# Performance work log

Hardware: AMD Instinct MI355X
Metric: run time of the kernel (lower is better)

## Reference

```python
import jax, jax.numpy as jnp
import numpy as np

HEADS = 16

def setup_inputs() -> dict:
    key = jax.random.key(0)
    ks = jax.random.split(key, 5)
    B, N, C = 2, 2048, 1024
    s = 0.02
    return {
        "x": jax.random.normal(ks[0], (B, N, C), jnp.float32),
        "y": jax.random.normal(ks[1], (B, N, C), jnp.float32),
        "w_qkv": jax.random.normal(ks[2], (C, 3 * C), jnp.float32) * s,  # acts as Linear weight^T
        "w_proj": jax.random.normal(ks[3], (C, C), jnp.float32) * s,
        "b_proj": jnp.zeros((C,), jnp.float32),
    }

def _qkv_heads(t, w_qkv, B, N, H, D):
    qkv = (t @ w_qkv).reshape(B, N, 3, H, D)
    qkv = jnp.transpose(qkv, (2, 0, 3, 1, 4))  # [3, B, H, N, D]
    return qkv[0], qkv[1], qkv[2]

def reference(x, y, w_qkv, w_proj, b_proj):
    B, N, C = x.shape
    H = HEADS
    D = C // H
    scale = D ** (-0.5)
    q, k, v = _qkv_heads(x, w_qkv, B, N, H, D)
    q1, k1, v1 = _qkv_heads(y, w_qkv, B, N, H, D)
    attn = jax.nn.softmax(jnp.einsum('bhnd,bhmd->bhnm', q, k) * scale, axis=-1)
    attn1 = jax.nn.softmax(jnp.einsum('bhnd,bhmd->bhnm', q1, k1) * scale, axis=-1)
    # cross-swapped values: x-branch attends over v1 (from y), y-branch over v (from x)
    ox = jnp.einsum('bhnm,bhmd->bhnd', attn, v1)
    oy = jnp.einsum('bhnm,bhmd->bhnd', attn1, v)
    ox = jnp.transpose(ox, (0, 2, 1, 3)).reshape(B, N, C)
    oy = jnp.transpose(oy, (0, 2, 1, 3)).reshape(B, N, C)
    x_out = ox @ w_proj + b_proj + x
    y_out = oy @ w_proj + b_proj + y
    return x_out, y_out
```

## Files before the change

kernel.cpp:

```cpp
#include <hip/hip_runtime.h>

using u16    = unsigned short;
using short8 = __attribute__((ext_vector_type(8))) short;
using f32x4  = __attribute__((ext_vector_type(4))) float;

#define MFMA16(a, b, c) __builtin_amdgcn_mfma_f32_16x16x32_bf16(a, b, c, 0, 0, 0)

#define QSCALE 0.18033688011112042f

__device__ inline u16 f2bf(float f) {
  union { float f; unsigned u; } v; v.f = f;
  unsigned r = v.u + 0x7fffu + ((v.u >> 16) & 1u);
  return (u16)(r >> 16);
}

__device__ __forceinline__ void load_lds16(const u16* g, u16* l) {
  __builtin_amdgcn_global_load_lds((const __attribute__((address_space(1))) void*)g,
                                   (__attribute__((address_space(3))) void*)l, 16, 0, 0);
}

__global__ __launch_bounds__(256) void cvt_k(const float* __restrict__ src,
                                             u16* __restrict__ dst) {
  const int i = (blockIdx.x * 256 + threadIdx.x) * 8;
  const float4 a = *(const float4*)&src[i];
  const float4 b = *(const float4*)&src[i + 4];
  short8 o;
  o[0] = (short)f2bf(a.x); o[1] = (short)f2bf(a.y);
  o[2] = (short)f2bf(a.z); o[3] = (short)f2bf(a.w);
  o[4] = (short)f2bf(b.x); o[5] = (short)f2bf(b.y);
  o[6] = (short)f2bf(b.z); o[7] = (short)f2bf(b.w);
  *(short8*)&dst[i] = o;
}

__global__ __launch_bounds__(256) void cvtT_k(const float* __restrict__ src,
                                              u16* __restrict__ dst, int R, int C) {
  __shared__ float t[64][65];
  const int c0 = blockIdx.x * 64, r0 = blockIdx.y * 64;
  const int lc = threadIdx.x & 63, g = threadIdx.x >> 6;
#pragma unroll
  for (int i = 0; i < 16; ++i) {
    const int r = g + i * 4;
    t[r][lc] = src[(size_t)(r0 + r) * C + c0 + lc];
  }
  __syncthreads();
#pragma unroll
  for (int i = 0; i < 16; ++i) {
    const int c = g + i * 4;
    dst[(size_t)(c0 + c) * R + r0 + lc] = f2bf(t[lc][c]);
  }
}

template <int MODE>
__global__ __launch_bounds__(256, 2) void gemm_k(
    const u16* __restrict__ A, const u16* __restrict__ Bt,
    u16* __restrict__ q_out, u16* __restrict__ k_out, u16* __restrict__ v_out,
    float* __restrict__ c_out, const float* __restrict__ bias,
    const float* __restrict__ res, int head_base) {
  __shared__ alignas(16) u16 lA[128 * 64];
  __shared__ alignas(16) u16 lB[128 * 64];
  const int tid = threadIdx.x;
  const int lane = tid & 63, wave = tid >> 6;
  const int quad = lane >> 4, l16 = lane & 15;
  const int lsw = (l16 & 7) * 8;
  const int wm = (wave >> 1) * 64, wn = (wave & 1) * 64;
  const int bn0 = blockIdx.x * 128, bm0 = blockIdx.y * 128;
  const int srow = lane >> 3;
  const int sg = (lane & 7) ^ srow;

  f32x4 acc[4][4] = {};

  for (int k0 = 0; k0 < 1024; k0 += 64) {
    __syncthreads();
#pragma unroll
    for (int it = 0; it < 4; ++it) {
      const int rb = wave * 32 + it * 8;
      const int r = rb + srow;
      load_lds16(&A[(size_t)(bm0 + r) * 1024 + k0 + sg * 8], &lA[rb * 64]);
      load_lds16(&Bt[(size_t)(bn0 + r) * 1024 + k0 + sg * 8], &lB[rb * 64]);
    }
    asm volatile("s_waitcnt vmcnt(0)" ::: "memory");
    __syncthreads();
#pragma unroll
    for (int kt = 0; kt < 2; ++kt) {
      short8 af[4], bfr[4];
#pragma unroll
      for (int i = 0; i < 4; ++i) {
        const int go = ((kt * 4 + quad) * 8) ^ lsw;
        af[i]  = *(const short8*)&lA[(wm + i * 16 + l16) * 64 + go];
        bfr[i] = *(const short8*)&lB[(wn + i * 16 + l16) * 64 + go];
      }
#pragma unroll
      for (int i = 0; i < 4; ++i)
#pragma unroll
        for (int j = 0; j < 4; ++j)
          acc[i][j] = MFMA16(af[i], bfr[j], acc[i][j]);
    }
  }

#pragma unroll
  for (int i = 0; i < 4; ++i) {
    const int row = bm0 + wm + i * 16 + quad * 4;
#pragma unroll
    for (int j = 0; j < 4; ++j) {
      const int col = bn0 + wn + j * 16 + l16;
#pragma unroll
      for (int r = 0; r < 4; ++r) {
        const float v = acc[i][j][r];
        const int m = row + r;
        if (MODE == 0) {
          const int which = col >> 10;
          const int h = (col >> 6) & 15, d = col & 63;
          const int b = m >> 11, n = m & 2047;
          const size_t hh = (size_t)(head_base + b * 16 + h);
          if (which == 0)      q_out[(hh * 2048 + n) * 64 + d] = f2bf(v * QSCALE);
          else if (which == 1) k_out[(hh * 2048 + n) * 64 + d] = f2bf(v);
          else                 v_out[(hh * 64 + d) * 2048 + n] = f2bf(v);
        } else {
          const size_t idx = (size_t)m * 1024 + col;
          c_out[idx] = v + bias[col] + res[idx];
        }
      }
    }
  }
}

__global__ __launch_bounds__(256, 2) void attn_k(const u16* __restrict__ Q,
                                                 const u16* __restrict__ K,
                                                 const u16* __restrict__ V,
                                                 u16* __restrict__ O) {
  __shared__ alignas(16) u16 kT[64 * 64];
  __shared__ alignas(16) u16 vT[64 * 64];
  __shared__ alignas(16) u16 pT[4][16 * 72];

  const int tid = threadIdx.x;
  const int lane = tid & 63, wave = tid >> 6;
  const int quad = lane >> 4, l16 = lane & 15;
  const int lsw = (l16 & 7) * 8;
  const int s = blockIdx.z >> 1, b = blockIdx.z & 1, h = blockIdx.y;
  const int head_qk = (s * 2 + b) * 16 + h;
  const int head_v  = ((1 - s) * 2 + b) * 16 + h;
  const u16* Qh = Q + (size_t)head_qk * 2048 * 64;
  const u16* Kh = K + (size_t)head_qk * 2048 * 64;
  const u16* Vh = V + (size_t)head_v * 64 * 2048;
  const int qr0 = blockIdx.x * 64 + wave * 16;

  short8 qf[2];
  qf[0] = *(const short8*)&Qh[(size_t)(qr0 + l16) * 64 + quad * 8];
  qf[1] = *(const short8*)&Qh[(size_t)(qr0 + l16) * 64 + 32 + quad * 8];

  f32x4 oacc[4] = {};
  float l_i = 0.f;

  const int srow = lane >> 3;
  const int sg = (lane & 7) ^ srow;

  union PU { uint2 u[2]; short8 s; };

  for (int j0 = 0; j0 < 2048; j0 += 64) {
    __syncthreads();
#pragma unroll
    for (int it = 0; it < 2; ++it) {
      const int rb = wave * 16 + it * 8;
      const int r = rb + srow;
      load_lds16(&Kh[(size_t)(j0 + r) * 64 + sg * 8], &kT[rb * 64]);
      load_lds16(&Vh[(size_t)r * 2048 + j0 + sg * 8], &vT[rb * 64]);
    }
    asm volatile("s_waitcnt vmcnt(0)" ::: "memory");
    __syncthreads();

    f32x4 sacc[4] = {};
#pragma unroll
    for (int kd = 0; kd < 2; ++kd)
#pragma unroll
      for (int kt = 0; kt < 4; ++kt) {
        const int go = ((kd * 4 + quad) * 8) ^ lsw;
        const short8 kf = *(const short8*)&kT[(kt * 16 + l16) * 64 + go];
        sacc[kt] = MFMA16(kf, qf[kd], sacc[kt]);
      }

    float p[4][4];
    float rs = 0.f;
#pragma unroll
    for (int kt = 0; kt < 4; ++kt) {
      float t0 = 0.f;
#pragma unroll
      for (int r = 0; r < 4; ++r) { p[kt][r] = exp2f(sacc[kt][r]); t0 += p[kt][r]; }
      rs += t0;
    }
    rs += __shfl_xor(rs, 16, 64);
    rs += __shfl_xor(rs, 32, 64);
    l_i += rs;

#pragma unroll
    for (int kt = 0; kt < 4; ++kt) {
      const unsigned lo = __builtin_amdgcn_perm(__float_as_uint(p[kt][1]),
                                                __float_as_uint(p[kt][0]), 0x07060302u);
      const unsigned hi = __builtin_amdgcn_perm(__float_as_uint(p[kt][3]),
                                                __float_as_uint(p[kt][2]), 0x07060302u);
      uint2 w; w.x = lo; w.y = hi;
      *(uint2*)&pT[wave][l16 * 72 + kt * 16 + quad * 4] = w;
    }

    asm volatile("s_waitcnt lgkmcnt(0)" ::: "memory");

    PU p0, p1;
    p0.u[0] = *(const uint2*)&pT[wave][l16 * 72 + quad * 8];
    p0.u[1] = *(const uint2*)&pT[wave][l16 * 72 + quad * 8 + 4];
    p1.u[0] = *(const uint2*)&pT[wave][l16 * 72 + 32 + quad * 8];
    p1.u[1] = *(const uint2*)&pT[wave][l16 * 72 + 32 + quad * 8 + 4];

#pragma unroll
    for (int nt = 0; nt < 4; ++nt) {
      const int go0 = (quad * 8) ^ lsw;
      const int go1 = ((4 + quad) * 8) ^ lsw;
      const short8 vf0 = *(const short8*)&vT[(nt * 16 + l16) * 64 + go0];
      const short8 vf1 = *(const short8*)&vT[(nt * 16 + l16) * 64 + go1];
      oacc[nt] = MFMA16(p0.s, vf0, oacc[nt]);
      oacc[nt] = MFMA16(p1.s, vf1, oacc[nt]);
    }
  }

  u16* Ob = O + (size_t)s * 4096 * 1024;
#pragma unroll
  for (int r = 0; r < 4; ++r) {
    const float lr = __shfl(l_i, quad * 4 + r, 64);
    const float inv = 1.f / lr;
    const int n = qr0 + quad * 4 + r;
#pragma unroll
    for (int nt = 0; nt < 4; ++nt)
      Ob[(size_t)(b * 2048 + n) * 1024 + h * 64 + nt * 16 + l16] = f2bf(oacc[nt][r] * inv);
  }
}

extern "C" void kernel_launch(void* const* d_in, const int* in_sizes, int n_in,
                              void* d_out, int out_size, void* d_ws, size_t ws_size,
                              hipStream_t stream) {
  const float* x      = (const float*)d_in[0];
  const float* y      = (const float*)d_in[1];
  const float* w_qkv  = (const float*)d_in[2];
  const float* w_proj = (const float*)d_in[3];
  const float* b_proj = (const float*)d_in[4];
  float* out = (float*)d_out;

  u16* xb     = (u16*)d_ws;
  u16* yb     = xb + 4194304;
  u16* Ob     = xb;
  u16* wqkvT  = yb + 4194304;
  u16* wprojT = wqkvT + 3145728;
  u16* Qs     = wprojT + 1048576;
  u16* Ks     = Qs + 8388608;
  u16* Vs     = Ks + 8388608;

  cvt_k<<<2048, 256, 0, stream>>>(x, xb);
  cvt_k<<<2048, 256, 0, stream>>>(y, yb);
  cvtT_k<<<dim3(48, 16), 256, 0, stream>>>(w_qkv, wqkvT, 1024, 3072);
  cvtT_k<<<dim3(16, 16), 256, 0, stream>>>(w_proj, wprojT, 1024, 1024);

  gemm_k<0><<<dim3(24, 32), 256, 0, stream>>>(xb, wqkvT, Qs, Ks, Vs,
                                              nullptr, nullptr, nullptr, 0);
  gemm_k<0><<<dim3(24, 32), 256, 0, stream>>>(yb, wqkvT, Qs, Ks, Vs,
                                              nullptr, nullptr, nullptr, 32);

  attn_k<<<dim3(32, 16, 4), 256, 0, stream>>>(Qs, Ks, Vs, Ob);

  gemm_k<1><<<dim3(8, 32), 256, 0, stream>>>(Ob, wprojT, nullptr, nullptr, nullptr,
                                             out, b_proj, x, 0);
  gemm_k<1><<<dim3(8, 32), 256, 0, stream>>>(Ob + 4194304, wprojT, nullptr, nullptr,
                                             nullptr, out + 4194304, b_proj, y, 0);
}
```

Measured before the change: 327.9 us.

## Switch attention to 32x32 MFMA with 32-row waves and merge GEMM launches

The attention kernel now uses 32x32x16 bf16 MFMA instructions, and each wave handles 32 query rows, so a block covers 128 rows and the grid is halved. This gives more reuse per K/V tile loaded into LDS and fewer LDS fragment reads per FLOP. Occupancy hint raised to 4 blocks per CU. Separately, the paired x/y GEMM launches are merged into single launches using blockIdx.z, which cuts launch count and fills the GPU better. The costs are higher register pressure from 16-wide accumulators and a larger P staging buffer.

```diff
diff --git a/kernel.cpp b/kernel.cpp
--- a/kernel.cpp
+++ b/kernel.cpp
@@ -3,8 +3,10 @@
 using u16    = unsigned short;
 using short8 = __attribute__((ext_vector_type(8))) short;
 using f32x4  = __attribute__((ext_vector_type(4))) float;
+using f32x16 = __attribute__((ext_vector_type(16))) float;
 
 #define MFMA16(a, b, c) __builtin_amdgcn_mfma_f32_16x16x32_bf16(a, b, c, 0, 0, 0)
+#define MFMA32(a, b, c) __builtin_amdgcn_mfma_f32_32x32x16_bf16(a, b, c, 0, 0, 0)
 
 #define QSCALE 0.18033688011112042f
 
@@ -52,12 +54,20 @@
 
 template <int MODE>
 __global__ __launch_bounds__(256, 2) void gemm_k(
-    const u16* __restrict__ A, const u16* __restrict__ Bt,
+    const u16* __restrict__ A0, const u16* __restrict__ A1,
+    const u16* __restrict__ Bt,
     u16* __restrict__ q_out, u16* __restrict__ k_out, u16* __restrict__ v_out,
-    float* __restrict__ c_out, const float* __restrict__ bias,
-    const float* __restrict__ res, int head_base) {
+    float* __restrict__ c0, float* __restrict__ c1,
+    const float* __restrict__ bias,
+    const float* __restrict__ res0, const float* __restrict__ res1) {
   __shared__ alignas(16) u16 lA[128 * 64];
   __shared__ alignas(16) u16 lB[128 * 64];
+  const int z = blockIdx.z;
+  const u16* A = z ? A1 : A0;
+  float* c_out = z ? c1 : c0;
+  const float* res = z ? res1 : res0;
+  const int head_base = z * 32;
+
   const int tid = threadIdx.x;
   const int lane = tid & 63, wave = tid >> 6;
   const int quad = lane >> 4, l16 = lane & 15;
@@ -124,31 +134,31 @@
   }
 }
 
-__global__ __launch_bounds__(256, 2) void attn_k(const u16* __restrict__ Q,
+__global__ __launch_bounds__(256, 4) void attn_k(const u16* __restrict__ Q,
                                                  const u16* __restrict__ K,
                                                  const u16* __restrict__ V,
                                                  u16* __restrict__ O) {
   __shared__ alignas(16) u16 kT[64 * 64];
   __shared__ alignas(16) u16 vT[64 * 64];
-  __shared__ alignas(16) u16 pT[4][16 * 72];
+  __shared__ alignas(16) u16 pT[4][32 * 72];
 
   const int tid = threadIdx.x;
   const int lane = tid & 63, wave = tid >> 6;
-  const int quad = lane >> 4, l16 = lane & 15;
-  const int lsw = (l16 & 7) * 8;
-  const int s = blockIdx.z >> 1, b = blockIdx.z & 1, h = blockIdx.y;
-  const int head_qk = (s * 2 + b) * 16 + h;
-  const int head_v  = ((1 - s) * 2 + b) * 16 + h;
+  const int qn = lane & 31, h = lane >> 5;
+  const int s = blockIdx.z >> 1, b = blockIdx.z & 1, hh = blockIdx.y;
+  const int head_qk = (s * 2 + b) * 16 + hh;
+  const int head_v  = ((1 - s) * 2 + b) * 16 + hh;
   const u16* Qh = Q + (size_t)head_qk * 2048 * 64;
   const u16* Kh = K + (size_t)head_qk * 2048 * 64;
   const u16* Vh = V + (size_t)head_v * 64 * 2048;
-  const int qr0 = blockIdx.x * 64 + wave * 16;
-
-  short8 qf[2];
-  qf[0] = *(const short8*)&Qh[(size_t)(qr0 + l16) * 64 + quad * 8];
-  qf[1] = *(const short8*)&Qh[(size_t)(qr0 + l16) * 64 + 32 + quad * 8];
-
-  f32x4 oacc[4] = {};
+  const int qr0 = blockIdx.x * 128 + wave * 32;
+
+  short8 qf[4];
+#pragma unroll
+  for (int f = 0; f < 4; ++f)
+    qf[f] = *(const short8*)&Qh[(size_t)(qr0 + qn) * 64 + f * 16 + h * 8];
+
+  f32x16 oacc[2] = {};
   float l_i = 0.f;
 
   const int srow = lane >> 3;
@@ -168,67 +178,73 @@
     asm volatile("s_waitcnt vmcnt(0)" ::: "memory");
     __syncthreads();
 
-    f32x4 sacc[4] = {};
-#pragma unroll
-    for (int kd = 0; kd < 2; ++kd)
-#pragma unroll
-      for (int kt = 0; kt < 4; ++kt) {
-        const int go = ((kd * 4 + quad) * 8) ^ lsw;
-        const short8 kf = *(const short8*)&kT[(kt * 16 + l16) * 64 + go];
-        sacc[kt] = MFMA16(kf, qf[kd], sacc[kt]);
-      }
-
-    float p[4][4];
+    f32x16 sacc[2] = {};
+#pragma unroll
+    for (int t = 0; t < 2; ++t) {
+      const int row = t * 32 + qn;
+      const int rsw = (row & 7);
+#pragma unroll
+      for (int kd = 0; kd < 4; ++kd) {
+        const int go = ((kd * 2 + h) ^ rsw) * 8;
+        const short8 kf = *(const short8*)&kT[row * 64 + go];
+        sacc[t] = MFMA32(kf, qf[kd], sacc[t]);
+      }
+    }
+
+    float p[2][16];
     float rs = 0.f;
 #pragma unroll
-    for (int kt = 0; kt < 4; ++kt) {
-      float t0 = 0.f;
-#pragma unroll
-      for (int r = 0; r < 4; ++r) { p[kt][r] = exp2f(sacc[kt][r]); t0 += p[kt][r]; }
-      rs += t0;
-    }
-    rs += __shfl_xor(rs, 16, 64);
+    for (int t = 0; t < 2; ++t)
+#pragma unroll
+      for (int r = 0; r < 16; ++r) { p[t][r] = exp2f(sacc[t][r]); rs += p[t][r]; }
     rs += __shfl_xor(rs, 32, 64);
     l_i += rs;
 
 #pragma unroll
-    for (int kt = 0; kt < 4; ++kt) {
-      const unsigned lo = __builtin_amdgcn_perm(__float_as_uint(p[kt][1]),
-                                                __float_as_uint(p[kt][0]), 0x07060302u);
-      const unsigned hi = __builtin_amdgcn_perm(__float_as_uint(p[kt][3]),
-                                                __float_as_uint(p[kt][2]), 0x07060302u);
-      uint2 w; w.x = lo; w.y = hi;
-      *(uint2*)&pT[wave][l16 * 72 + kt * 16 + quad * 4] = w;
-    }
+    for (int t = 0; t < 2; ++t)
+#pragma unroll
+      for (int g = 0; g < 4; ++g) {
+        const int k0 = 32 * t + 8 * g + 4 * h;
+        uint2 w;
+        w.x = __builtin_amdgcn_perm(__float_as_uint(p[t][4 * g + 1]),
+                                    __float_as_uint(p[t][4 * g + 0]), 0x07060302u);
+        w.y = __builtin_amdgcn_perm(__float_as_uint(p[t][4 * g + 3]),
+                                    __float_as_uint(p[t][4 * g + 2]), 0x07060302u);
+        *(uint2*)&pT[wave][qn * 72 + k0] = w;
+      }
 
     asm volatile("s_waitcnt lgkmcnt(0)" ::: "memory");
 
-    PU p0, p1;
-    p0.u[0] = *(const uint2*)&pT[wave][l16 * 72 + quad * 8];
-    p0.u[1] = *(const uint2*)&pT[wave][l16 * 72 + quad * 8 + 4];
-    p1.u[0] = *(const uint2*)&pT[wave][l16 * 72 + 32 + quad * 8];
-    p1.u[1] = *(const uint2*)&pT[wave][l16 * 72 + 32 + quad * 8 + 4];
-
-#pragma unroll
-    for (int nt = 0; nt < 4; ++nt) {
-      const int go0 = (quad * 8) ^ lsw;
-      const int go1 = ((4 + quad) * 8) ^ lsw;
-      const short8 vf0 = *(const short8*)&vT[(nt * 16 + l16) * 64 + go0];
-      const short8 vf1 = *(const short8*)&vT[(nt * 16 + l16) * 64 + go1];
-      oacc[nt] = MFMA16(p0.s, vf0, oacc[nt]);
-      oacc[nt] = MFMA16(p1.s, vf1, oacc[nt]);
+    PU pa[4];
+#pragma unroll
+    for (int st = 0; st < 4; ++st) {
+      pa[st].u[0] = *(const uint2*)&pT[wave][qn * 72 + st * 16 + h * 8];
+      pa[st].u[1] = *(const uint2*)&pT[wave][qn * 72 + st * 16 + h * 8 + 4];
+    }
+
+#pragma unroll
+    for (int dt = 0; dt < 2; ++dt) {
+      const int row = dt * 32 + qn;
+      const int rsw = (row & 7);
+#pragma unroll
+      for (int st = 0; st < 4; ++st) {
+        const int go = ((st * 2 + h) ^ rsw) * 8;
+        const short8 vf = *(const short8*)&vT[row * 64 + go];
+        oacc[dt] = MFMA32(pa[st].s, vf, oacc[dt]);
+      }
     }
   }
 
   u16* Ob = O + (size_t)s * 4096 * 1024;
 #pragma unroll
-  for (int r = 0; r < 4; ++r) {
-    const float lr = __shfl(l_i, quad * 4 + r, 64);
+  for (int r = 0; r < 16; ++r) {
+    const int qrow = (r & 3) + 8 * (r >> 2) + 4 * h;
+    const float lr = __shfl(l_i, qrow, 64);
     const float inv = 1.f / lr;
-    const int n = qr0 + quad * 4 + r;
-#pragma unroll
-    for (int nt = 0; nt < 4; ++nt)
-      Ob[(size_t)(b * 2048 + n) * 1024 + h * 64 + nt * 16 + l16] = f2bf(oacc[nt][r] * inv);
+    const size_t base = (size_t)(b * 2048 + qr0 + qrow) * 1024 + hh * 64;
+#pragma unroll
+    for (int dt = 0; dt < 2; ++dt)
+      Ob[base + dt * 32 + qn] = f2bf(oacc[dt][r] * inv);
   }
 }
 
@@ -256,15 +272,13 @@
   cvtT_k<<<dim3(48, 16), 256, 0, stream>>>(w_qkv, wqkvT, 1024, 3072);
   cvtT_k<<<dim3(16, 16), 256, 0, stream>>>(w_proj, wprojT, 1024, 1024);
 
-  gemm_k<0><<<dim3(24, 32), 256, 0, stream>>>(xb, wqkvT, Qs, Ks, Vs,
-                                              nullptr, nullptr, nullptr, 0);
-  gemm_k<0><<<dim3(24, 32), 256, 0, stream>>>(yb, wqkvT, Qs, Ks, Vs,
-                                              nullptr, nullptr, nullptr, 32);
-
-  attn_k<<<dim3(32, 16, 4), 256, 0, stream>>>(Qs, Ks, Vs, Ob);
-
-  gemm_k<1><<<dim3(8, 32), 256, 0, stream>>>(Ob, wprojT, nullptr, nullptr, nullptr,
-                                             out, b_proj, x, 0);
-  gemm_k<1><<<dim3(8, 32), 256, 0, stream>>>(Ob + 4194304, wprojT, nullptr, nullptr,
-                                             nullptr, out + 4194304, b_proj, y, 0);
-}
+  gemm_k<0><<<dim3(24, 32, 2), 256, 0, stream>>>(xb, yb, wqkvT, Qs, Ks, Vs,
+                                                 nullptr, nullptr, nullptr,
+                                                 nullptr, nullptr);
+
+  attn_k<<<dim3(16, 16, 4), 256, 0, stream>>>(Qs, Ks, Vs, Ob);
+
+  gemm_k<1><<<dim3(8, 32, 2), 256, 0, stream>>>(Ob, Ob + 4194304, wprojT,
+                                                nullptr, nullptr, nullptr,
+                                                out, out + 4194304, b_proj, x, y);
+}
```

Measured after the change: 313.8 us. 1.05x faster.
